# Kernel optimization log

Measured on AMD Instinct MI355X. Metric: run time of the kernel, lower is better.

## Reference

```python
import jax, jax.numpy as jnp
import numpy as np
import math

BASE_RES = 16
MAX_RES = 2048
LEVELS = 16
FEAT_DIM = 2
LOG_B = math.log(MAX_RES / BASE_RES) / (LEVELS - 1)  # per-level log scale


def setup_inputs() -> dict:
    key = jax.random.key(0)
    k1, k2 = jax.random.split(key)
    B = 1048576
    positions = jax.random.uniform(k1, (B, 3), dtype=jnp.float32)
    total = MAX_RES * MAX_RES * 3 * FEAT_DIM
    # torch.nn.init.uniform_ -> U[0,1)
    plane_table = jax.random.uniform(k2, (total,), dtype=jnp.float32)
    return {"positions": positions, "plane_table": plane_table}


def _encode(positions, plane_table):
    B = positions.shape[0]
    dtype = positions.dtype
    # planes: (xy, yz, zx) -> [B, 3 planes, 2 coords]
    x, y, z = positions[:, 0], positions[:, 1], positions[:, 2]
    xyz6 = jnp.stack([x, y, y, z, z, x], axis=1).reshape(B, 3, 2)
    planes = plane_table.reshape(3, MAX_RES * MAX_RES, FEAT_DIM)
    plane_ids = jnp.arange(3)  # [3]
    outs = []
    for level in range(LEVELS):
        scale = BASE_RES * math.exp(level * LOG_B) - 1.0
        res = int(math.ceil(scale)) + 1  # grid_resolution
        pos = xyz6 * (res - 1) + 0.5            # [B,3,2]
        pg = jnp.floor(pos)
        frac = pos - pg                          # fractional part
        pg = pg.astype(jnp.int32)
        local = jnp.zeros((B, 3, FEAT_DIM), dtype)
        for idx in range(4):  # 4 bilinear corners
            w = jnp.ones((B, 3), dtype)
            coords = []
            for d in range(2):
                if idx & (1 << d):
                    coords.append(pg[..., d] + 1)
                    w = w * frac[..., d]
                else:
                    coords.append(pg[..., d])
                    w = w * (1.0 - frac[..., d])
            c = jnp.stack(coords, axis=-1).astype(dtype)  # [B,3,2]
            # remap corner from level grid to the max_res storage grid (truncating cast)
            c_ori = (c / res * (MAX_RES - 1)).astype(jnp.int32)
            index = c_ori[..., 0] + c_ori[..., 1] * MAX_RES  # [B,3] flat plane index
            feats = planes[plane_ids[None, :], index]        # [B,3,FEAT_DIM] gather
            local = local + w[..., None] * feats
        # cross-plane product
        outs.append(local[:, 0] * local[:, 1] * local[:, 2])  # [B,FEAT_DIM]
    out = jnp.stack(outs, axis=2)  # [B, FEAT_DIM, LEVELS]; sn = j*LEVELS + level
    return out.reshape(B, FEAT_DIM * LEVELS)


def reference(positions, plane_table):
    return _encode(positions, plane_table)
```

## Files before the change

### kernel.cpp

```cpp
#include <hip/hip_runtime.h>
#include <math.h>

#define LEVELS 16
#define MAX_RES 2048
#define NCELL_BITS 5
#define NCELLS (1 << (3 * NCELL_BITS))
#define LUT_MAX 8192

typedef float nfloat4 __attribute__((ext_vector_type(4)));

struct ResParams { int res[LEVELS]; int off[LEVELS]; int total; };


__global__ __launch_bounds__(256) void zero_hist(unsigned int* hist) {
  int i = blockIdx.x * 256 + threadIdx.x;
  if (i < NCELLS) hist[i] = 0u;
}

__device__ __forceinline__ unsigned int morton5(int cx, int cy, int cz) {
  unsigned int k = 0;
  #pragma unroll
  for (int b = 0; b < NCELL_BITS; ++b)
    k |= (((cx >> b) & 1) << (3 * b)) | (((cy >> b) & 1) << (3 * b + 1)) |
         (((cz >> b) & 1) << (3 * b + 2));
  return k;
}

__device__ __forceinline__ unsigned int cell_of(float x, float y, float z) {
  int cx = min(31, max(0, (int)(x * 32.0f)));
  int cy = min(31, max(0, (int)(y * 32.0f)));
  int cz = min(31, max(0, (int)(z * 32.0f)));
  return morton5(cx, cy, cz);
}

__global__ __launch_bounds__(256) void keys_hist(const float* __restrict__ pos,
                                                 unsigned int* __restrict__ hist, int B) {
  int i = blockIdx.x * 256 + threadIdx.x;
  if (i >= B) return;
  atomicAdd(&hist[cell_of(pos[i*3], pos[i*3+1], pos[i*3+2])], 1u);
}

__global__ __launch_bounds__(1024) void scan_kernel(const unsigned int* __restrict__ hist,
                                                    unsigned int* __restrict__ offs) {
  __shared__ unsigned int part[1024];
  const int SEG = NCELLS / 1024;
  int t = threadIdx.x;
  int base = t * SEG;
  unsigned int s = 0;
  #pragma unroll
  for (int j = 0; j < SEG; ++j) s += hist[base + j];
  part[t] = s;
  __syncthreads();
  for (int off = 1; off < 1024; off <<= 1) {
    unsigned int v = (t >= off) ? part[t - off] : 0u;
    __syncthreads();
    part[t] += v;
    __syncthreads();
  }
  unsigned int run = part[t] - s;
  #pragma unroll
  for (int j = 0; j < SEG; ++j) {
    unsigned int c = hist[base + j];
    offs[base + j] = run;
    run += c;
  }
}

__global__ __launch_bounds__(256) void scatter_kernel(const float* __restrict__ pos,
                                                      unsigned int* __restrict__ offs,
                                                      nfloat4* __restrict__ sorted, int B) {
  int i = blockIdx.x * 256 + threadIdx.x;
  if (i >= B) return;
  float x = pos[i*3], y = pos[i*3+1], z = pos[i*3+2];
  unsigned int slot = atomicAdd(&offs[cell_of(x, y, z)], 1u);
  nfloat4 v = {x, y, z, __int_as_float(i)};
  sorted[slot] = v;
}


__global__ __launch_bounds__(256) void triplane_main(
    const nfloat4* __restrict__ sorted,
    const float* __restrict__ table,
    float* __restrict__ out,
    ResParams P, int B, int nwg)
{
  int wg = blockIdx.x;
  int q = nwg >> 3, r = nwg & 7;
  int xcd = wg & 7, idx = wg >> 3;
  int swz = (xcd < r) ? xcd * (q + 1) + idx : r * (q + 1) + (xcd - r) * q + idx;
  int t = swz * 256 + (int)threadIdx.x;

  nfloat4 s = {0.f, 0.f, 0.f, 0.f};
  if (t < B) s = sorted[t];

  __shared__ unsigned short lut[LUT_MAX];
  for (int j = threadIdx.x; j < P.total; j += 256) {
    int l = 0;
    #pragma unroll
    for (int k = 1; k < LEVELS; ++k) if (j >= P.off[k]) l = k;
    int c = j - P.off[l];
    lut[j] = (unsigned short)(int)(__fmul_rn(__fdiv_rn((float)c, (float)P.res[l]), 2047.0f));
  }
  __syncthreads();
  if (t >= B) return;

  float x = s.x, y = s.y, z = s.z;
  int orig = __float_as_int(s.w);

  float uarr[3] = {x, y, z};
  float varr[3] = {y, z, x};

  float o0[LEVELS], o1[LEVELS];

  #pragma unroll
  for (int l = 0; l < LEVELS; ++l) {
    const float resm1 = (float)(P.res[l] - 1);
    const int   o     = P.off[l];

    float prod0 = 1.0f, prod1 = 1.0f;

    #pragma unroll
    for (int p = 0; p < 3; ++p) {
      float pu = __fadd_rn(__fmul_rn(uarr[p], resm1), 0.5f);
      float pv = __fadd_rn(__fmul_rn(varr[p], resm1), 0.5f);
      float gu = floorf(pu), gv = floorf(pv);
      float fu = __fsub_rn(pu, gu);
      float fv = __fsub_rn(pv, gv);
      int iu = (int)gu, iv = (int)gv;

      int cou0 = lut[o + iu];
      int cou1 = lut[o + iu + 1];
      int cov0 = lut[o + iv];
      int cov1 = lut[o + iv + 1];

      const float* plane = table + (size_t)p * (MAX_RES * MAX_RES * 2);

      const float2 f00 = *reinterpret_cast<const float2*>(plane + (size_t)(cou0 + (cov0 << 11)) * 2);
      const float2 f10 = *reinterpret_cast<const float2*>(plane + (size_t)(cou1 + (cov0 << 11)) * 2);
      const float2 f01 = *reinterpret_cast<const float2*>(plane + (size_t)(cou0 + (cov1 << 11)) * 2);
      const float2 f11 = *reinterpret_cast<const float2*>(plane + (size_t)(cou1 + (cov1 << 11)) * 2);

      float w00 = (1.0f - fu) * (1.0f - fv);
      float w10 = fu * (1.0f - fv);
      float w01 = (1.0f - fu) * fv;
      float w11 = fu * fv;

      float a0 = 0.0f, a1 = 0.0f;
      a0 += w00 * f00.x;  a1 += w00 * f00.y;
      a0 += w10 * f10.x;  a1 += w10 * f10.y;
      a0 += w01 * f01.x;  a1 += w01 * f01.y;
      a0 += w11 * f11.x;  a1 += w11 * f11.y;

      prod0 *= a0;
      prod1 *= a1;
    }

    o0[l] = prod0;
    o1[l] = prod1;
  }

  nfloat4* base = reinterpret_cast<nfloat4*>(out + (size_t)orig * 32);
  #pragma unroll
  for (int k = 0; k < 4; ++k) {
    nfloat4 v0 = {o0[k*4+0], o0[k*4+1], o0[k*4+2], o0[k*4+3]};
    nfloat4 v1 = {o1[k*4+0], o1[k*4+1], o1[k*4+2], o1[k*4+3]};
    base[k] = v0;
    base[4 + k] = v1;
  }
}

extern "C" void kernel_launch(void* const* d_in, const int* in_sizes, int n_in,
                              void* d_out, int out_size, void* d_ws, size_t ws_size,
                              hipStream_t stream) {
  const float* positions = (const float*)d_in[0];
  const float* table     = (const float*)d_in[1];
  float* out             = (float*)d_out;
  int B = in_sizes[0] / 3;

  ResParams P;
  const double LOG_B = log(2048.0 / 16.0) / (double)(LEVELS - 1);
  int run = 0;
  for (int l = 0; l < LEVELS; ++l) {
    double scale = 16.0 * exp((double)l * LOG_B) - 1.0;
    P.res[l] = (int)ceil(scale) + 1;
    P.off[l] = run;
    run += P.res[l] + 1;
  }
  P.total = run;

  int nwg = (B + 255) / 256;

  size_t off_hist   = 0;
  size_t off_offs   = off_hist + (size_t)NCELLS * 4;
  size_t off_sorted = off_offs + (size_t)NCELLS * 4;
  size_t need       = off_sorted + (size_t)B * 16;

  if (ws_size >= need && P.total <= LUT_MAX) {
    unsigned int* hist = (unsigned int*)((char*)d_ws + off_hist);
    unsigned int* offs = (unsigned int*)((char*)d_ws + off_offs);
    nfloat4*      srt  = (nfloat4*)((char*)d_ws + off_sorted);

    hipLaunchKernelGGL(zero_hist, dim3((NCELLS + 255) / 256), dim3(256), 0, stream, hist);
    hipLaunchKernelGGL(keys_hist, dim3(nwg), dim3(256), 0, stream, positions, hist, B);
    hipLaunchKernelGGL(scan_kernel, dim3(1), dim3(1024), 0, stream, hist, offs);
    hipLaunchKernelGGL(scatter_kernel, dim3(nwg), dim3(256), 0, stream, positions, offs, srt, B);
    hipLaunchKernelGGL(triplane_main, dim3(nwg), dim3(256), 0, stream,
                       srt, table, out, P, B, nwg);
  }
}
```

Measured before the change: 492.8 us.

## Replace shared-memory index LUT with verified float multiply and stream outputs per level group

Removes the per-block shared-memory lookup table and its __syncthreads. Corner indices are now computed on the fly with a per-level multiplier that the host checks to give the same truncated result as the divide-then-scale reference, falling back to an exact divide for levels where no multiplier matches. Levels are processed in reverse and each group of four is stored as soon as it completes, so the 32 output registers are no longer held to the end. This trades LDS traffic and setup for a few extra ALU ops, and adds an unsorted fallback path when the workspace is too small.

```diff
diff --git a/kernel.cpp b/kernel.cpp
--- a/kernel.cpp
+++ b/kernel.cpp
@@ -5,11 +5,10 @@
 #define MAX_RES 2048
 #define NCELL_BITS 5
 #define NCELLS (1 << (3 * NCELL_BITS))
-#define LUT_MAX 8192
 
 typedef float nfloat4 __attribute__((ext_vector_type(4)));
 
-struct ResParams { int res[LEVELS]; int off[LEVELS]; int total; };
+struct ResParams { int res[LEVELS]; float mul[LEVELS]; int mulmask; };
 
 
 __global__ __launch_bounds__(256) void zero_hist(unsigned int* hist) {
@@ -78,8 +77,10 @@
 }
 
 
+template <bool SORTED>
 __global__ __launch_bounds__(256) void triplane_main(
     const nfloat4* __restrict__ sorted,
+    const float* __restrict__ positions,
     const float* __restrict__ table,
     float* __restrict__ out,
     ResParams P, int B, int nwg)
@@ -89,33 +90,28 @@
   int xcd = wg & 7, idx = wg >> 3;
   int swz = (xcd < r) ? xcd * (q + 1) + idx : r * (q + 1) + (xcd - r) * q + idx;
   int t = swz * 256 + (int)threadIdx.x;
-
-  nfloat4 s = {0.f, 0.f, 0.f, 0.f};
-  if (t < B) s = sorted[t];
-
-  __shared__ unsigned short lut[LUT_MAX];
-  for (int j = threadIdx.x; j < P.total; j += 256) {
-    int l = 0;
-    #pragma unroll
-    for (int k = 1; k < LEVELS; ++k) if (j >= P.off[k]) l = k;
-    int c = j - P.off[l];
-    lut[j] = (unsigned short)(int)(__fmul_rn(__fdiv_rn((float)c, (float)P.res[l]), 2047.0f));
-  }
-  __syncthreads();
   if (t >= B) return;
 
-  float x = s.x, y = s.y, z = s.z;
-  int orig = __float_as_int(s.w);
+  float x, y, z; int orig;
+  if (SORTED) {
+    nfloat4 s = sorted[t];
+    x = s.x; y = s.y; z = s.z;
+    orig = __float_as_int(s.w);
+  } else {
+    x = positions[t*3]; y = positions[t*3+1]; z = positions[t*3+2];
+    orig = t;
+  }
 
   float uarr[3] = {x, y, z};
   float varr[3] = {y, z, x};
 
-  float o0[LEVELS], o1[LEVELS];
-
-  #pragma unroll
-  for (int l = 0; l < LEVELS; ++l) {
+  float g0[4], g1[4];
+  nfloat4* base = reinterpret_cast<nfloat4*>(out + (size_t)orig * 32);
+
+  #pragma unroll
+  for (int li = 0; li < LEVELS; ++li) {
+    const int l = LEVELS - 1 - li;
     const float resm1 = (float)(P.res[l] - 1);
-    const int   o     = P.off[l];
 
     float prod0 = 1.0f, prod1 = 1.0f;
 
@@ -126,12 +122,23 @@
       float gu = floorf(pu), gv = floorf(pv);
       float fu = __fsub_rn(pu, gu);
       float fv = __fsub_rn(pv, gv);
-      int iu = (int)gu, iv = (int)gv;
-
-      int cou0 = lut[o + iu];
-      int cou1 = lut[o + iu + 1];
-      int cov0 = lut[o + iv];
-      int cov1 = lut[o + iv + 1];
+      float gu1 = __fadd_rn(gu, 1.0f);
+      float gv1 = __fadd_rn(gv, 1.0f);
+
+      int cou0, cou1, cov0, cov1;
+      if ((P.mulmask >> l) & 1) {
+        const float m = P.mul[l];
+        cou0 = (int)__fmul_rn(gu,  m);
+        cou1 = (int)__fmul_rn(gu1, m);
+        cov0 = (int)__fmul_rn(gv,  m);
+        cov1 = (int)__fmul_rn(gv1, m);
+      } else {
+        const float fres = (float)P.res[l];
+        cou0 = (int)(__fmul_rn(__fdiv_rn(gu,  fres), 2047.0f));
+        cou1 = (int)(__fmul_rn(__fdiv_rn(gu1, fres), 2047.0f));
+        cov0 = (int)(__fmul_rn(__fdiv_rn(gv,  fres), 2047.0f));
+        cov1 = (int)(__fmul_rn(__fdiv_rn(gv1, fres), 2047.0f));
+      }
 
       const float* plane = table + (size_t)p * (MAX_RES * MAX_RES * 2);
 
@@ -155,17 +162,15 @@
       prod1 *= a1;
     }
 
-    o0[l] = prod0;
-    o1[l] = prod1;
-  }
-
-  nfloat4* base = reinterpret_cast<nfloat4*>(out + (size_t)orig * 32);
-  #pragma unroll
-  for (int k = 0; k < 4; ++k) {
-    nfloat4 v0 = {o0[k*4+0], o0[k*4+1], o0[k*4+2], o0[k*4+3]};
-    nfloat4 v1 = {o1[k*4+0], o1[k*4+1], o1[k*4+2], o1[k*4+3]};
-    base[k] = v0;
-    base[4 + k] = v1;
+    g0[l & 3] = prod0;
+    g1[l & 3] = prod1;
+
+    if ((l & 3) == 0) {
+      nfloat4 v0 = {g0[0], g0[1], g0[2], g0[3]};
+      nfloat4 v1 = {g1[0], g1[1], g1[2], g1[3]};
+      base[l >> 2]     = v0;
+      base[4 + (l >> 2)] = v1;
+    }
   }
 }
 
@@ -178,15 +183,28 @@
   int B = in_sizes[0] / 3;
 
   ResParams P;
+  P.mulmask = 0;
   const double LOG_B = log(2048.0 / 16.0) / (double)(LEVELS - 1);
-  int run = 0;
   for (int l = 0; l < LEVELS; ++l) {
     double scale = 16.0 * exp((double)l * LOG_B) - 1.0;
-    P.res[l] = (int)ceil(scale) + 1;
-    P.off[l] = run;
-    run += P.res[l] + 1;
-  }
-  P.total = run;
+    int res = (int)ceil(scale) + 1;
+    P.res[l] = res;
+    P.mul[l] = 0.0f;
+    float fres = (float)res;
+    float m0 = (float)(2047.0 / (double)res);
+    float cands[3] = { m0, nextafterf(m0, 3.4e38f), nextafterf(m0, 0.0f) };
+    for (int ci = 0; ci < 3; ++ci) {
+      bool ok = true;
+      for (int c = 0; c <= res; ++c) {
+        volatile float cf = (float)c;
+        volatile float qq = cf / fres;
+        volatile float rr = qq * 2047.0f;
+        volatile float rc = cf * cands[ci];
+        if ((int)rr != (int)rc) { ok = false; break; }
+      }
+      if (ok) { P.mul[l] = cands[ci]; P.mulmask |= (1 << l); break; }
+    }
+  }
 
   int nwg = (B + 255) / 256;
 
@@ -195,7 +213,7 @@
   size_t off_sorted = off_offs + (size_t)NCELLS * 4;
   size_t need       = off_sorted + (size_t)B * 16;
 
-  if (ws_size >= need && P.total <= LUT_MAX) {
+  if (ws_size >= need) {
     unsigned int* hist = (unsigned int*)((char*)d_ws + off_hist);
     unsigned int* offs = (unsigned int*)((char*)d_ws + off_offs);
     nfloat4*      srt  = (nfloat4*)((char*)d_ws + off_sorted);
@@ -204,7 +222,10 @@
     hipLaunchKernelGGL(keys_hist, dim3(nwg), dim3(256), 0, stream, positions, hist, B);
     hipLaunchKernelGGL(scan_kernel, dim3(1), dim3(1024), 0, stream, hist, offs);
     hipLaunchKernelGGL(scatter_kernel, dim3(nwg), dim3(256), 0, stream, positions, offs, srt, B);
-    hipLaunchKernelGGL(triplane_main, dim3(nwg), dim3(256), 0, stream,
-                       srt, table, out, P, B, nwg);
-  }
-}
+    hipLaunchKernelGGL((triplane_main<true>), dim3(nwg), dim3(256), 0, stream,
+                       srt, positions, table, out, P, B, nwg);
+  } else {
+    hipLaunchKernelGGL((triplane_main<false>), dim3(nwg), dim3(256), 0, stream,
+                       (const nfloat4*)nullptr, positions, table, out, P, B, nwg);
+  }
+}
```

New measurement: 509.5 us. +3.4%, slower.
